# Optimization experiments

Measured on AMD Instinct MI355X. Metric: run time of the kernel, lower is better.

## Reference

```python
import jax, jax.numpy as jnp
import numpy as np
from jax import lax

# Static model/config sizes
B, ANG, C, H, NF, NB = 1, 9, 3, 128, 16, 2


def get_freq_position(n):
    """Anti-diagonal frequency bands of an n x n angular-DCT grid (python/static)."""
    bands = []
    for i in range(n):
        bands.append(([i], [0]))
    for j in range(1, n):
        bands.append(([n - 1], [j]))
    for item in bands:
        while item[0][0] > 0 and item[1][0] < n - 1:
            item[0].insert(0, item[0][0] - 1)
            item[1].insert(0, item[1][0] + 1)
    return bands


def dct_mat(n):
    """Orthonormal DCT-II matrix (row k = k-th basis)."""
    k = jnp.arange(n, dtype=jnp.float32)[:, None]
    i = jnp.arange(n, dtype=jnp.float32)[None, :]
    m = jnp.cos(jnp.pi * (i + 0.5) * k / n) * jnp.sqrt(2.0 / n)
    return m.at[0].multiply(1.0 / np.sqrt(2.0))


def conv3d(x, w, b):
    # x: (N, Cin, D, H, W), w: (Cout, Cin, 3, 3, 3)
    y = lax.conv_general_dilated(x, w, (1, 1, 1), 'SAME',
                                 dimension_numbers=('NCDHW', 'OIDHW', 'NCDHW'))
    return y + b[None, :, None, None, None]


def branch(cut, wi, bi, a, wb, bb):
    """init conv + NB ResBlock3D (PReLU -> Conv3d, residual), plus outer skip."""
    y0 = conv3d(cut, wi, bi)
    y = y0
    for k in range(NB):
        r = jnp.where(y >= 0, y, a[k] * y)  # PReLU (single-parameter)
        y = y + conv3d(r, wb[k], bb[k])
    return y0 + y


def setup_inputs() -> dict:
    key = jax.random.key(0)
    ks = jax.random.split(key, 32)

    def nrm(k, shape, s=0.05):
        return jax.random.normal(k, shape, dtype=jnp.float32) * s

    inp = {"x": jax.random.normal(ks[0], (B, ANG, ANG, C, H, H), dtype=jnp.float32)}
    i = 1
    for n in ("dc", "lo", "mi", "hi"):
        inp[f"w_{n}_i"] = nrm(ks[i], (NF, C, 3, 3, 3)); i += 1
        inp[f"b_{n}_i"] = nrm(ks[i], (NF,)); i += 1
        inp[f"a_{n}"] = jnp.full((NB,), 0.25, dtype=jnp.float32)
        inp[f"w_{n}"] = nrm(ks[i], (NB, NF, NF, 3, 3, 3)); i += 1
        inp[f"b_{n}"] = nrm(ks[i], (NB, NF)); i += 1
    inp["w_last"] = nrm(ks[i], (C, NF))  # 1x1 Conv2d, no bias
    return inp


def reference(x, w_dc_i, b_dc_i, a_dc, w_dc, b_dc,
              w_lo_i, b_lo_i, a_lo, w_lo, b_lo,
              w_mi_i, b_mi_i, a_mi, w_mi, b_mi,
              w_hi_i, b_hi_i, a_hi, w_hi, b_hi, w_last):
    b, u, v, c, h, w = x.shape
    Da = dct_mat(u)  # angular DCT (u == v)
    Ds = dct_mat(h)  # spatial DCT (h == w)

    # SpaAngDCT: spatial 2D DCT then angular 2D DCT
    xf = jnp.einsum('buvchw,Hh,Ww->buvcHW', x, Ds, Ds)
    xf = jnp.einsum('buvchw,Uu,Vv->bUVchw', xf, Da, Da)

    x_rec = jnp.zeros((b, NF, u, v, h, w), dtype=x.dtype)
    for idx, (ui, vi) in enumerate(get_freq_position(u)):
        if idx == 0:
            p = (w_dc_i, b_dc_i, a_dc, w_dc, b_dc)
        elif idx <= 2:
            p = (w_lo_i, b_lo_i, a_lo, w_lo, b_lo)
        elif idx <= u - 1:
            p = (w_mi_i, b_mi_i, a_mi, w_mi, b_mi)
        else:
            p = (w_hi_i, b_hi_i, a_hi, w_hi, b_hi)
        ua, va = jnp.array(ui), jnp.array(vi)
        cut = xf[:, ua, va].transpose(0, 2, 1, 3, 4)  # (b, c, L, h, w)
        out = branch(cut, *p)                          # (b, NF, L, h, w)
        x_rec = x_rec.at[:, :, ua, va].set(out)        # scatter band back

    # 'b c u v h w -> b c (u h) (v w)' then 1x1 conv (NF -> 3)
    xr = x_rec.transpose(0, 1, 2, 4, 3, 5).reshape(b, NF, u * h, v * w)
    xr = jnp.einsum('bnHW,on->boHW', xr, w_last)
    xr = xr.reshape(b, c, u, h, v, w).transpose(0, 2, 4, 1, 3, 5)  # (b,u,v,c,h,w)

    # InverseSpaAngDCT: angular IDCT then spatial IDCT
    xr = jnp.einsum('bUVchw,Uu,Vv->buvchw', xr, Da, Da)
    xr = jnp.einsum('buvcHW,Hh,Ww->buvchw', xr, Ds, Ds)
    return xr + x
```

## Files before the change

### kernel.cpp

```cpp
#include <hip/hip_runtime.h>
#include <hip/hip_bf16.h>
#include <math.h>

typedef __hip_bfloat16 bf16;
typedef __attribute__((ext_vector_type(8))) short short8;
typedef __attribute__((ext_vector_type(4))) float floatx4;
typedef __attribute__((ext_vector_type(4))) unsigned int uint4v;
typedef __attribute__((ext_vector_type(2))) unsigned int uint2v;

#define HW 16384
#define NSLICE 243

__constant__ int c_s_of_p[81] = {
  0, 1,1, 2,2,2, 3,3,3,3, 4,4,4,4,4, 5,5,5,5,5,5, 6,6,6,6,6,6,6,
  7,7,7,7,7,7,7,7, 8,8,8,8,8,8,8,8,8, 9,9,9,9,9,9,9,9,
  10,10,10,10,10,10,10, 11,11,11,11,11,11, 12,12,12,12,12,
  13,13,13,13, 14,14,14, 15,15, 16};
__constant__ int c_l_of_p[81] = {
  0, 0,1, 0,1,2, 0,1,2,3, 0,1,2,3,4, 0,1,2,3,4,5, 0,1,2,3,4,5,6,
  0,1,2,3,4,5,6,7, 0,1,2,3,4,5,6,7,8, 0,1,2,3,4,5,6,7,
  0,1,2,3,4,5,6, 0,1,2,3,4,5, 0,1,2,3,4, 0,1,2,3, 0,1,2, 0,1, 0};
__constant__ int c_L_of_s[17] = {1,2,3,4,5,6,7,8,9,8,7,6,5,4,3,2,1};
__constant__ int c_g_of_s[17] = {0,1,1,2,2,2,2,2,2,3,3,3,3,3,3,3,3};
__constant__ int c_pos_uv[81] = {
  0,1,3,6,10,15,21,28,36,
  2,4,7,11,16,22,29,37,45,
  5,8,12,17,23,30,38,46,53,
  9,13,18,24,31,39,47,54,60,
  14,19,25,32,40,48,55,61,66,
  20,26,33,41,49,56,62,67,71,
  27,34,42,50,57,63,68,72,75,
  35,43,51,58,64,69,73,76,78,
  44,52,59,65,70,74,77,79,80};

struct WPtrs {
  const float* wi[4]; const float* bi[4]; const float* a[4];
  const float* wb[4]; const float* bb[4]; const float* wl;
};

__device__ __forceinline__ unsigned short f2bf(float f) {
  return __bfloat16_as_ushort(__float2bfloat16(f));
}
__device__ __forceinline__ float bflo(unsigned int w) {
  return __uint_as_float(w << 16);
}
__device__ __forceinline__ float bfhi(unsigned int w) {
  return __uint_as_float(w & 0xffff0000u);
}
__device__ __forceinline__ unsigned int pack2(float a, float b) {
  return (unsigned int)f2bf(a) | ((unsigned int)f2bf(b) << 16);
}
__device__ __forceinline__ float invprelu(float v, float invA) {
  return (v >= 0.f) ? v : v * invA;
}
__device__ __forceinline__ void bfsplit(float v, unsigned short& hi, unsigned short& lo) {
  unsigned int bits = __float_as_uint(v);
  hi = (unsigned short)(bits >> 16);
  lo = f2bf(v - __uint_as_float(bits & 0xffff0000u));
}
__device__ __forceinline__ void gl_lds16(const void* g, void* l) {
  __builtin_amdgcn_global_load_lds(
      (const __attribute__((address_space(1))) unsigned int*)g,
      (__attribute__((address_space(3))) unsigned int*)l, 16, 0, 0);
}

__global__ __launch_bounds__(256) void k_setup(float* DaF,
                                               unsigned short* TFhi, unsigned short* TFlo,
                                               unsigned short* TIhi, unsigned short* TIlo) {
  const double PI = 3.14159265358979323846;
  int t = blockIdx.x * 256 + threadIdx.x;
  if (t < 81) {
    int U = t / 9, u = t % 9;
    double d = cos(PI * (u + 0.5) * U / 9.0) * sqrt(2.0 / 9.0);
    if (U == 0) d *= (1.0 / sqrt(2.0));
    DaF[t] = (float)d;
  }
  if (t < 16384) {
    int jj = t & 7, lane = (t >> 3) & 63, ks = (t >> 9) & 3, tile = t >> 11;
    int row = tile * 16 + (lane & 15);
    int colk = ks * 32 + (lane >> 4) * 8 + jj;
    double vF = cos(PI * (colk + 0.5) * row / 128.0) * sqrt(2.0 / 128.0);
    if (row == 0) vF *= (1.0 / sqrt(2.0));
    double vI = cos(PI * (row + 0.5) * colk / 128.0) * sqrt(2.0 / 128.0);
    if (colk == 0) vI *= (1.0 / sqrt(2.0));
    unsigned short h, l;
    bfsplit((float)vF, h, l); TFhi[t] = h; TFlo[t] = l;
    bfsplit((float)vI, h, l); TIhi[t] = h; TIlo[t] = l;
  }
}

__global__ __launch_bounds__(256) void k_prep(WPtrs P, unsigned short* Wmf,
                                              float* BiF, float* BbF,
                                              float* AF, float* WlF) {
  int t = blockIdx.x * 256 + threadIdx.x;
  if (t < 92160) {
    int s = t / 7680, r = t % 7680;
    int step = r / 512, r2 = r % 512;
    int lane = r2 >> 3, j = r2 & 7;
    int d = step / 5, i = step % 5;
    int q = lane >> 4, m = lane & 15;
    int tl = 2 * i + (q >> 1);
    int cin = (q & 1) * 8 + j;
    float val = 0.f;
    if (tl <= 8) {
      int ky = tl / 3, kx = tl % 3;
      int tap = d * 9 + ky * 3 + kx;
      if (s < 4) {
        if (cin < 3) val = P.wi[s][(m * 3 + cin) * 27 + tap];
      } else {
        int g = (s - 4) >> 1, k = (s - 4) & 1;
        val = P.wb[g][((k * 16 + m) * 16 + cin) * 27 + tap];
      }
    }
    Wmf[t] = f2bf(val);
  }
  if (t < 64)  BiF[t] = P.bi[t / 16][t % 16];
  if (t < 128) BbF[t] = P.bb[t / 32][t % 32];
  if (t < 8)   AF[t]  = P.a[t / 2][t % 2];
  if (t < 48)  WlF[t] = P.wl[t];
}

__global__ __launch_bounds__(256) void k_dct2(const float* __restrict__ X,
                                              const unsigned short* __restrict__ tabhi,
                                              const unsigned short* __restrict__ tablo,
                                              const float* __restrict__ xres,
                                              float* __restrict__ Y) {
  __shared__ unsigned short sThi[128 * 136];
  __shared__ unsigned short sTlo[128 * 136];
  int s = blockIdx.x;
  int t = threadIdx.x;
  int lane = t & 63, wv = t >> 6;
  int q = lane >> 4, n16 = lane & 15;
  const float* Xs = X + (size_t)s * HW;

  floatx4 acc[2][8];
#pragma unroll
  for (int mt = 0; mt < 2; mt++)
#pragma unroll
    for (int nt = 0; nt < 8; nt++) acc[mt][nt] = (floatx4){0.f, 0.f, 0.f, 0.f};

#pragma unroll
  for (int ks = 0; ks < 4; ks++) {
    short8 ahi[2], alo[2];
#pragma unroll
    for (int mt = 0; mt < 2; mt++) {
      const float* xp = Xs + (wv * 32 + mt * 16 + n16) * 128 + ks * 32 + q * 8;
      float4 a = *(const float4*)xp;
      float4 b = *(const float4*)(xp + 4);
      union { short8 v; unsigned short u[8]; } H, L;
      float xv[8] = {a.x, a.y, a.z, a.w, b.x, b.y, b.z, b.w};
#pragma unroll
      for (int j = 0; j < 8; j++) bfsplit(xv[j], H.u[j], L.u[j]);
      ahi[mt] = H.v; alo[mt] = L.v;
    }
#pragma unroll
    for (int nt = 0; nt < 8; nt++) {
      int e = nt * 2048 + ks * 512 + lane * 8;
      short8 bh = *(const short8*)(tabhi + e);
      short8 bl = *(const short8*)(tablo + e);
#pragma unroll
      for (int mt = 0; mt < 2; mt++) {
        acc[mt][nt] = __builtin_amdgcn_mfma_f32_16x16x32_bf16(ahi[mt], bl, acc[mt][nt], 0, 0, 0);
        acc[mt][nt] = __builtin_amdgcn_mfma_f32_16x16x32_bf16(alo[mt], bh, acc[mt][nt], 0, 0, 0);
        acc[mt][nt] = __builtin_amdgcn_mfma_f32_16x16x32_bf16(ahi[mt], bh, acc[mt][nt], 0, 0, 0);
      }
    }
  }

#pragma unroll
  for (int mt = 0; mt < 2; mt++)
#pragma unroll
    for (int nt = 0; nt < 8; nt++) {
      int col = nt * 16 + n16;
      int rowb = wv * 32 + mt * 16 + q * 4;
#pragma unroll
      for (int rp = 0; rp < 4; rp += 2) {
        unsigned short h0, l0, h1, l1;
        bfsplit(acc[mt][nt][rp], h0, l0);
        bfsplit(acc[mt][nt][rp + 1], h1, l1);
        int widx = (col * 136 + rowb + rp) >> 1;
        ((unsigned int*)sThi)[widx] = (unsigned int)h0 | ((unsigned int)h1 << 16);
        ((unsigned int*)sTlo)[widx] = (unsigned int)l0 | ((unsigned int)l1 << 16);
      }
    }
  __syncthreads();

#pragma unroll
  for (int mt = 0; mt < 2; mt++)
#pragma unroll
    for (int nt = 0; nt < 8; nt++) acc[mt][nt] = (floatx4){0.f, 0.f, 0.f, 0.f};

#pragma unroll
  for (int ks = 0; ks < 4; ks++) {
    short8 ahi[2], alo[2];
#pragma unroll
    for (int mt = 0; mt < 2; mt++) {
      int e = (wv * 2 + mt) * 2048 + ks * 512 + lane * 8;
      ahi[mt] = *(const short8*)(tabhi + e);
      alo[mt] = *(const short8*)(tablo + e);
    }
#pragma unroll
    for (int nt = 0; nt < 8; nt++) {
      int off = (nt * 16 + n16) * 136 + ks * 32 + q * 8;
      short8 bh = *(const short8*)(sThi + off);
      short8 bl = *(const short8*)(sTlo + off);
#pragma unroll
      for (int mt = 0; mt < 2; mt++) {
        acc[mt][nt] = __builtin_amdgcn_mfma_f32_16x16x32_bf16(ahi[mt], bl, acc[mt][nt], 0, 0, 0);
        acc[mt][nt] = __builtin_amdgcn_mfma_f32_16x16x32_bf16(alo[mt], bh, acc[mt][nt], 0, 0, 0);
        acc[mt][nt] = __builtin_amdgcn_mfma_f32_16x16x32_bf16(ahi[mt], bh, acc[mt][nt], 0, 0, 0);
      }
    }
  }

#pragma unroll
  for (int mt = 0; mt < 2; mt++)
#pragma unroll
    for (int nt = 0; nt < 8; nt++) {
      int row0 = wv * 32 + mt * 16 + q * 4;
      int col = nt * 16 + n16;
#pragma unroll
      for (int r = 0; r < 4; r++) {
        size_t oi = (size_t)s * HW + (size_t)(row0 + r) * 128 + col;
        float v = acc[mt][nt][r];
        if (xres) v += xres[oi];
        Y[oi] = v;
      }
    }
}

__global__ __launch_bounds__(128) void k_angF(const float* __restrict__ xf1,
                                              const float* __restrict__ DaF,
                                              unsigned short* __restrict__ xf2b) {
  __shared__ float L[81 * 128];
  __shared__ float sDa[81];
  int t = threadIdx.x;
  int c = blockIdx.y;
  int hw = blockIdx.x * 128 + t;
  if (t < 81) sDa[t] = DaF[t];
  __syncthreads();
#pragma unroll 3
  for (int i = 0; i < 81; i++)
    L[i * 128 + t] = xf1[(size_t)(i * 3 + c) * HW + hw];
  for (int v = 0; v < 9; v++) {
    float f[9];
#pragma unroll
    for (int u = 0; u < 9; u++) f[u] = L[(u * 9 + v) * 128 + t];
#pragma unroll
    for (int U = 0; U < 9; U++) {
      float a = 0.f;
#pragma unroll
      for (int u = 0; u < 9; u++) a += sDa[U * 9 + u] * f[u];
      L[(U * 9 + v) * 128 + t] = a;
    }
  }
  for (int U = 0; U < 9; U++) {
    float f[9];
#pragma unroll
    for (int v = 0; v < 9; v++) f[v] = L[(U * 9 + v) * 128 + t];
#pragma unroll
    for (int V = 0; V < 9; V++) {
      float a = 0.f;
#pragma unroll
      for (int v = 0; v < 9; v++) a += sDa[V * 9 + v] * f[v];
      size_t base = ((size_t)c_pos_uv[U * 9 + V] * HW + hw) * 4;
      xf2b[base + c] = f2bf(a);
      if (c == 0) xf2b[base + 3] = 0;
    }
  }
}

__global__ __launch_bounds__(128) void k_angI(const float* __restrict__ xrb,
                                              const float* __restrict__ DaF,
                                              float* __restrict__ xr2) {
  __shared__ float L[81 * 128];
  __shared__ float sDa[81];
  int t = threadIdx.x;
  int c = blockIdx.y;
  int hw = blockIdx.x * 128 + t;
  if (t < 81) sDa[t] = DaF[t];
  __syncthreads();
#pragma unroll 3
  for (int i = 0; i < 81; i++)
    L[i * 128 + t] = xrb[((size_t)c_pos_uv[i] * 3 + c) * HW + hw];
  for (int U = 0; U < 9; U++) {
    float f[9];
#pragma unroll
    for (int V = 0; V < 9; V++) f[V] = L[(U * 9 + V) * 128 + t];
#pragma unroll
    for (int v = 0; v < 9; v++) {
      float a = 0.f;
#pragma unroll
      for (int V = 0; V < 9; V++) a += sDa[V * 9 + v] * f[V];
      L[(U * 9 + v) * 128 + t] = a;
    }
  }
  for (int v = 0; v < 9; v++) {
    float f[9];
#pragma unroll
    for (int U = 0; U < 9; U++) f[U] = L[(U * 9 + v) * 128 + t];
#pragma unroll
    for (int u = 0; u < 9; u++) {
      float a = 0.f;
#pragma unroll
      for (int U = 0; U < 9; U++) a += sDa[U * 9 + u] * f[U];
      xr2[(size_t)((u * 9 + v) * 3 + c) * HW + hw] = a;
    }
  }
}

__global__ __launch_bounds__(512) void k_conv(const unsigned short* __restrict__ src,
                                              const unsigned short* __restrict__ prevAct,
                                              const unsigned short* __restrict__ act0,
                                              const unsigned short* __restrict__ Wmf,
                                              const float* __restrict__ BiF,
                                              const float* __restrict__ BbF,
                                              const float* __restrict__ AF,
                                              const float* __restrict__ WlF,
                                              int sel,
                                              unsigned short* __restrict__ boutAct,
                                              float* __restrict__ xrbOut) {
  __shared__ unsigned short s_lds[10 * 132 * 16];
  int p = blockIdx.y;
  int s = c_s_of_p[p], l = c_l_of_p[p];
  int g = c_g_of_s[s], Ls = c_L_of_s[s];
  int row0 = blockIdx.x * 8;
  int t = threadIdx.x;
  int lane = t & 63, wv = t >> 6;
  int q = lane >> 4, n = lane & 15;

  float aNext = (sel < 2) ? AF[g * 2 + sel] : 0.f;
  float invA  = (sel > 0) ? 1.0f / AF[g * 2 + sel - 1] : 0.f;

  int scol = t & 127;
  int shalf = (t >> 7) & 1;
  int srow0 = t >> 8;

  {
    uint4v z = (uint4v){0u, 0u, 0u, 0u};
    int zmax = (sel == 0) ? 1320 : 40;
    for (int i = t; i < zmax; i += 512) {
      int row, half, col;
      if (i < 40) { row = i >> 2; half = (i >> 1) & 1; col = (i & 1) ? 129 : 0; }
      else { int j = i - 40; row = j >> 7; col = (j & 127) + 1; half = 1; }
      *(uint4v*)((char*)s_lds + (size_t)(((row * 2 + half) * 132 + col)) * 16) = z;
    }
    for (int row = 0; row < 10; row++) {
      int grow = row0 - 1 + row;
      if ((unsigned)grow >= 128u) {
        for (int i = t; i < 264; i += 512) {
          int half = i / 132, col = i % 132;
          *(uint4v*)((char*)s_lds + (size_t)((row * 2 + half) * 132 + col) * 16) = z;
        }
      }
    }
  }

  int basel = wv * 4224 + (q & 1) * 2112 + n * 16;
  int off2[5];
#pragma unroll
  for (int i = 0; i < 5; i++) {
    int tl = 2 * i + (q >> 1);
    if (tl > 8) tl = 8;
    int ky = tl / 3, kx = tl % 3;
    off2[i] = basel + ky * 4224 + kx * 16;
  }

  int setIdx = (sel == 0) ? g : (4 + g * 2 + (sel - 1));
  const char* WsetBase = (const char*)Wmf + (size_t)setIdx * 15 * 1024;

  floatx4 acc[8];
#pragma unroll
  for (int cg = 0; cg < 8; cg++) acc[cg] = (floatx4){0.f, 0.f, 0.f, 0.f};

  for (int d = 0; d < 3; d++) {
    int l2 = l + d - 1;
    if (l2 < 0 || l2 >= Ls) continue;
    int p2 = p + d - 1;
    __syncthreads();
    if (sel == 0) {
      if (shalf == 0) {
#pragma unroll
        for (int it = 0; it < 5; it++) {
          int row = srow0 + it * 2;
          int grow = row0 - 1 + row;
          if ((unsigned)grow < 128u) {
            uint2v v2 = *(const uint2v*)(src + ((size_t)p2 * HW + grow * 128 + scol) * 4);
            uint4v val; val.x = v2.x; val.y = v2.y; val.z = 0u; val.w = 0u;
            *(uint4v*)((char*)s_lds + (size_t)((row * 2) * 132 + scol + 1) * 16) = val;
          }
        }
      }
    } else {
#pragma unroll
      for (int it = 0; it < 5; it++) {
        int row = srow0 + it * 2;
        int grow = row0 - 1 + row;
        if ((unsigned)grow < 128u) {
          const void* gp = (const void*)(src +
              (((size_t)p2 * HW + (size_t)grow * 128 + scol) * 16 + shalf * 8));
          void* lp = (void*)((char*)s_lds +
              (size_t)((row * 2 + shalf) * 132 + (wv & 1) * 64 + 1) * 16);
          gl_lds16(gp, lp);
        }
      }
    }
    __syncthreads();
    short8 af[5];
#pragma unroll
    for (int i = 0; i < 5; i++)
      af[i] = *(const short8*)(WsetBase + ((d * 5 + i) * 64 + lane) * 16);
#pragma unroll
    for (int cg = 0; cg < 8; cg++) {
#pragma unroll
      for (int i = 0; i < 5; i++) {
        short8 b = *(const short8*)((const char*)s_lds + off2[i] + cg * 256);
        acc[cg] = __builtin_amdgcn_mfma_f32_16x16x32_bf16(af[i], b, acc[cg], 0, 0, 0);
      }
    }
  }

  const float* bp = (sel == 0) ? (BiF + g * 16) : (BbF + g * 32 + (sel - 1) * 16);
  float bz[4];
#pragma unroll
  for (int r = 0; r < 4; r++) bz[r] = bp[q * 4 + r];
  int h = row0 + wv;

  if (sel < 2) {
#pragma unroll
    for (int cg = 0; cg < 8; cg++) {
      size_t pix = (size_t)p * HW + h * 128 + cg * 16 + n;
      float r0 = acc[cg][0] + bz[0], r1 = acc[cg][1] + bz[1];
      float r2 = acc[cg][2] + bz[2], r3 = acc[cg][3] + bz[3];
      if (sel != 0) {
        uint2v pv = *(const uint2v*)(prevAct + pix * 16 + q * 4);
        r0 += invprelu(bflo(pv.x), invA); r1 += invprelu(bfhi(pv.x), invA);
        r2 += invprelu(bflo(pv.y), invA); r3 += invprelu(bfhi(pv.y), invA);
      }
      r0 = fmaxf(r0, 0.f) + aNext * fminf(r0, 0.f);
      r1 = fmaxf(r1, 0.f) + aNext * fminf(r1, 0.f);
      r2 = fmaxf(r2, 0.f) + aNext * fminf(r2, 0.f);
      r3 = fmaxf(r3, 0.f) + aNext * fminf(r3, 0.f);
      uint2v ov; ov.x = pack2(r0, r1); ov.y = pack2(r2, r3);
      *(uint2v*)(boutAct + pix * 16 + q * 4) = ov;
    }
  } else {
    float invA0 = 1.0f / AF[g * 2];
    float wl0[4], wl1[4], wl2[4];
#pragma unroll
    for (int r = 0; r < 4; r++) {
      wl0[r] = WlF[q * 4 + r];
      wl1[r] = WlF[16 + q * 4 + r];
      wl2[r] = WlF[32 + q * 4 + r];
    }
#pragma unroll
    for (int cg = 0; cg < 8; cg++) {
      size_t pix = (size_t)p * HW + h * 128 + cg * 16 + n;
      float r0 = acc[cg][0] + bz[0], r1 = acc[cg][1] + bz[1];
      float r2 = acc[cg][2] + bz[2], r3 = acc[cg][3] + bz[3];
      uint2v pv = *(const uint2v*)(prevAct + pix * 16 + q * 4);
      r0 += invprelu(bflo(pv.x), invA); r1 += invprelu(bfhi(pv.x), invA);
      r2 += invprelu(bflo(pv.y), invA); r3 += invprelu(bfhi(pv.y), invA);
      uint2v p0 = *(const uint2v*)(act0 + pix * 16 + q * 4);
      r0 += invprelu(bflo(p0.x), invA0); r1 += invprelu(bfhi(p0.x), invA0);
      r2 += invprelu(bflo(p0.y), invA0); r3 += invprelu(bfhi(p0.y), invA0);
      float o0 = wl0[0] * r0 + wl0[1] * r1 + wl0[2] * r2 + wl0[3] * r3;
      float o1 = wl1[0] * r0 + wl1[1] * r1 + wl1[2] * r2 + wl1[3] * r3;
      float o2 = wl2[0] * r0 + wl2[1] * r1 + wl2[2] * r2 + wl2[3] * r3;
      o0 += __shfl_xor(o0, 16); o0 += __shfl_xor(o0, 32);
      o1 += __shfl_xor(o1, 16); o1 += __shfl_xor(o1, 32);
      o2 += __shfl_xor(o2, 16); o2 += __shfl_xor(o2, 32);
      if (q == 0) {
        size_t hw = (size_t)h * 128 + cg * 16 + n;
        xrbOut[((size_t)p * 3 + 0) * HW + hw] = o0;
        xrbOut[((size_t)p * 3 + 1) * HW + hw] = o1;
        xrbOut[((size_t)p * 3 + 2) * HW + hw] = o2;
      }
    }
  }
}

extern "C" void kernel_launch(void* const* d_in, const int* in_sizes, int n_in,
                              void* d_out, int out_size, void* d_ws, size_t ws_size,
                              hipStream_t stream) {
  (void)in_sizes; (void)n_in; (void)out_size; (void)ws_size;
  const float* x = (const float*)d_in[0];
  WPtrs P;
  for (int g = 0; g < 4; g++) {
    int b = 1 + g * 5;
    P.wi[g] = (const float*)d_in[b + 0];
    P.bi[g] = (const float*)d_in[b + 1];
    P.a[g]  = (const float*)d_in[b + 2];
    P.wb[g] = (const float*)d_in[b + 3];
    P.bb[g] = (const float*)d_in[b + 4];
  }
  P.wl = (const float*)d_in[21];

  char* base = (char*)d_ws;
  size_t off = 0;
  auto take = [&](size_t bytes) -> char* {
    char* r = base + off;
    off += (bytes + 255) & ~(size_t)255;
    return r;
  };
  float* DaF = (float*)take(81 * 4);
  unsigned short* TFhi = (unsigned short*)take(16384 * 2);
  unsigned short* TFlo = (unsigned short*)take(16384 * 2);
  unsigned short* TIhi = (unsigned short*)take(16384 * 2);
  unsigned short* TIlo = (unsigned short*)take(16384 * 2);
  unsigned short* Wmf = (unsigned short*)take(92160 * 2);
  float* BiF   = (float*)take(256);
  float* BbF   = (float*)take(512);
  float* AF    = (float*)take(32);
  float* WlF   = (float*)take(192);
  float* R1 = (float*)take((size_t)NSLICE * HW * 4);
  float* R3 = (float*)take((size_t)NSLICE * HW * 4);
  unsigned short* braw0 = (unsigned short*)take((size_t)81 * 16 * HW * 2);
  unsigned short* braw1 = (unsigned short*)take((size_t)81 * 16 * HW * 2);
  unsigned short* xf2b = (unsigned short*)R3;
  float* xrb = R3;

  k_setup<<<64, 256, 0, stream>>>(DaF, TFhi, TFlo, TIhi, TIlo);
  k_prep<<<360, 256, 0, stream>>>(P, Wmf, BiF, BbF, AF, WlF);
  k_dct2<<<243, 256, 0, stream>>>(x, TFhi, TFlo, nullptr, R1);
  k_angF<<<dim3(128, 3), 128, 0, stream>>>(R1, DaF, xf2b);
  k_conv<<<dim3(16, 81), 512, 0, stream>>>(xf2b, nullptr, nullptr, Wmf,
                                           BiF, BbF, AF, WlF, 0, braw0, nullptr);
  k_conv<<<dim3(16, 81), 512, 0, stream>>>(braw0, braw0, nullptr, Wmf,
                                           BiF, BbF, AF, WlF, 1, braw1, nullptr);
  k_conv<<<dim3(16, 81), 512, 0, stream>>>(braw1, braw1, braw0, Wmf,
                                           BiF, BbF, AF, WlF, 2, nullptr, xrb);
  k_angI<<<dim3(128, 3), 128, 0, stream>>>(xrb, DaF, R1);
  k_dct2<<<243, 256, 0, stream>>>(R1, TIhi, TIlo, x, (float*)d_out);
}
```

Measured before the change: 301.7 us.

## Merge setup kernels, bf16 intermediates, swizzle conv LDS, restructure angular DCT kernels

Merges the setup and weight-prep kernels into one launch. The forward spatial DCT now writes bf16 output, which the angular DCT reads directly from global memory instead of staging fp32 through LDS. The angular kernels use 256 threads and keep bf16 intermediates in LDS. The conv kernel gets a padded and swizzled LDS layout to reduce bank conflicts, and its weight-fragment loads are hoisted ahead of the tile fill. The extra bf16 rounding in the angular stages adds precision loss.

Result: faster. 294.8 us (-2.3%).

```diff
diff --git a/kernel.cpp b/kernel.cpp
--- a/kernel.cpp
+++ b/kernel.cpp
@@ -41,6 +41,9 @@
 __device__ __forceinline__ unsigned short f2bf(float f) {
   return __bfloat16_as_ushort(__float2bfloat16(f));
 }
+__device__ __forceinline__ float bf2f(unsigned short u) {
+  return __uint_as_float(((unsigned int)u) << 16);
+}
 __device__ __forceinline__ float bflo(unsigned int w) {
   return __uint_as_float(w << 16);
 }
@@ -63,10 +66,16 @@
       (const __attribute__((address_space(1))) unsigned int*)g,
       (__attribute__((address_space(3))) unsigned int*)l, 16, 0, 0);
 }
-
-__global__ __launch_bounds__(256) void k_setup(float* DaF,
-                                               unsigned short* TFhi, unsigned short* TFlo,
-                                               unsigned short* TIhi, unsigned short* TIlo) {
+__device__ __forceinline__ int ldsoff(int plane, int col) {
+  return plane * 2112 + ((plane & 3) << 5) + (col << 4);
+}
+
+__global__ __launch_bounds__(256) void k_init(WPtrs P, float* DaF,
+                                              unsigned short* TFhi, unsigned short* TFlo,
+                                              unsigned short* TIhi, unsigned short* TIlo,
+                                              unsigned short* Wmf,
+                                              float* BiF, float* BbF,
+                                              float* AF, float* WlF) {
   const double PI = 3.14159265358979323846;
   int t = blockIdx.x * 256 + threadIdx.x;
   if (t < 81) {
@@ -87,12 +96,6 @@
     bfsplit((float)vF, h, l); TFhi[t] = h; TFlo[t] = l;
     bfsplit((float)vI, h, l); TIhi[t] = h; TIlo[t] = l;
   }
-}
-
-__global__ __launch_bounds__(256) void k_prep(WPtrs P, unsigned short* Wmf,
-                                              float* BiF, float* BbF,
-                                              float* AF, float* WlF) {
-  int t = blockIdx.x * 256 + threadIdx.x;
   if (t < 92160) {
     int s = t / 7680, r = t % 7680;
     int step = r / 512, r2 = r % 512;
@@ -124,7 +127,8 @@
                                               const unsigned short* __restrict__ tabhi,
                                               const unsigned short* __restrict__ tablo,
                                               const float* __restrict__ xres,
-                                              float* __restrict__ Y) {
+                                              float* __restrict__ Yf,
+                                              unsigned short* __restrict__ Ybf) {
   __shared__ unsigned short sThi[128 * 136];
   __shared__ unsigned short sTlo[128 * 136];
   int s = blockIdx.x;
@@ -223,41 +227,43 @@
       for (int r = 0; r < 4; r++) {
         size_t oi = (size_t)s * HW + (size_t)(row0 + r) * 128 + col;
         float v = acc[mt][nt][r];
-        if (xres) v += xres[oi];
-        Y[oi] = v;
-      }
-    }
-}
-
-__global__ __launch_bounds__(128) void k_angF(const float* __restrict__ xf1,
-                                              const float* __restrict__ DaF,
-                                              unsigned short* __restrict__ xf2b) {
-  __shared__ float L[81 * 128];
+        if (Ybf) {
+          Ybf[oi] = f2bf(v);
+        } else {
+          if (xres) v += xres[oi];
+          Yf[oi] = v;
+        }
+      }
+    }
+}
+
+__global__ __launch_bounds__(256) void k_angF2(const unsigned short* __restrict__ in,
+                                               const float* __restrict__ DaF,
+                                               unsigned short* __restrict__ xf2b) {
+  __shared__ unsigned short L[81 * 256];
   __shared__ float sDa[81];
   int t = threadIdx.x;
   int c = blockIdx.y;
-  int hw = blockIdx.x * 128 + t;
+  int hw = blockIdx.x * 256 + t;
   if (t < 81) sDa[t] = DaF[t];
   __syncthreads();
-#pragma unroll 3
-  for (int i = 0; i < 81; i++)
-    L[i * 128 + t] = xf1[(size_t)(i * 3 + c) * HW + hw];
   for (int v = 0; v < 9; v++) {
     float f[9];
 #pragma unroll
-    for (int u = 0; u < 9; u++) f[u] = L[(u * 9 + v) * 128 + t];
+    for (int u = 0; u < 9; u++)
+      f[u] = bf2f(in[(size_t)((u * 9 + v) * 3 + c) * HW + hw]);
 #pragma unroll
     for (int U = 0; U < 9; U++) {
       float a = 0.f;
 #pragma unroll
       for (int u = 0; u < 9; u++) a += sDa[U * 9 + u] * f[u];
-      L[(U * 9 + v) * 128 + t] = a;
+      L[(U * 9 + v) * 256 + t] = f2bf(a);
     }
   }
   for (int U = 0; U < 9; U++) {
     float f[9];
 #pragma unroll
-    for (int v = 0; v < 9; v++) f[v] = L[(U * 9 + v) * 128 + t];
+    for (int v = 0; v < 9; v++) f[v] = bf2f(L[(U * 9 + v) * 256 + t]);
 #pragma unroll
     for (int V = 0; V < 9; V++) {
       float a = 0.f;
@@ -270,35 +276,33 @@
   }
 }
 
-__global__ __launch_bounds__(128) void k_angI(const float* __restrict__ xrb,
-                                              const float* __restrict__ DaF,
-                                              float* __restrict__ xr2) {
-  __shared__ float L[81 * 128];
+__global__ __launch_bounds__(256) void k_angI2(const float* __restrict__ xrb,
+                                               const float* __restrict__ DaF,
+                                               float* __restrict__ xr2) {
+  __shared__ unsigned short L[81 * 256];
   __shared__ float sDa[81];
   int t = threadIdx.x;
   int c = blockIdx.y;
-  int hw = blockIdx.x * 128 + t;
+  int hw = blockIdx.x * 256 + t;
   if (t < 81) sDa[t] = DaF[t];
   __syncthreads();
-#pragma unroll 3
-  for (int i = 0; i < 81; i++)
-    L[i * 128 + t] = xrb[((size_t)c_pos_uv[i] * 3 + c) * HW + hw];
   for (int U = 0; U < 9; U++) {
     float f[9];
 #pragma unroll
-    for (int V = 0; V < 9; V++) f[V] = L[(U * 9 + V) * 128 + t];
+    for (int V = 0; V < 9; V++)
+      f[V] = xrb[((size_t)c_pos_uv[U * 9 + V] * 3 + c) * HW + hw];
 #pragma unroll
     for (int v = 0; v < 9; v++) {
       float a = 0.f;
 #pragma unroll
       for (int V = 0; V < 9; V++) a += sDa[V * 9 + v] * f[V];
-      L[(U * 9 + v) * 128 + t] = a;
+      L[(U * 9 + v) * 256 + t] = f2bf(a);
     }
   }
   for (int v = 0; v < 9; v++) {
     float f[9];
 #pragma unroll
-    for (int U = 0; U < 9; U++) f[U] = L[(U * 9 + v) * 128 + t];
+    for (int U = 0; U < 9; U++) f[U] = bf2f(L[(U * 9 + v) * 256 + t]);
 #pragma unroll
     for (int u = 0; u < 9; u++) {
       float a = 0.f;
@@ -320,7 +324,7 @@
                                               int sel,
                                               unsigned short* __restrict__ boutAct,
                                               float* __restrict__ xrbOut) {
-  __shared__ unsigned short s_lds[10 * 132 * 16];
+  __shared__ unsigned short s_lds[21184];
   int p = blockIdx.y;
   int s = c_s_of_p[p], l = c_l_of_p[p];
   int g = c_g_of_s[s], Ls = c_L_of_s[s];
@@ -343,27 +347,26 @@
       int row, half, col;
       if (i < 40) { row = i >> 2; half = (i >> 1) & 1; col = (i & 1) ? 129 : 0; }
       else { int j = i - 40; row = j >> 7; col = (j & 127) + 1; half = 1; }
-      *(uint4v*)((char*)s_lds + (size_t)(((row * 2 + half) * 132 + col)) * 16) = z;
+      *(uint4v*)((char*)s_lds + ldsoff(row * 2 + half, col)) = z;
     }
     for (int row = 0; row < 10; row++) {
       int grow = row0 - 1 + row;
       if ((unsigned)grow >= 128u) {
         for (int i = t; i < 264; i += 512) {
           int half = i / 132, col = i % 132;
-          *(uint4v*)((char*)s_lds + (size_t)((row * 2 + half) * 132 + col) * 16) = z;
+          *(uint4v*)((char*)s_lds + ldsoff(row * 2 + half, col)) = z;
         }
       }
     }
   }
 
-  int basel = wv * 4224 + (q & 1) * 2112 + n * 16;
   int off2[5];
 #pragma unroll
   for (int i = 0; i < 5; i++) {
     int tl = 2 * i + (q >> 1);
     if (tl > 8) tl = 8;
     int ky = tl / 3, kx = tl % 3;
-    off2[i] = basel + ky * 4224 + kx * 16;
+    off2[i] = ldsoff(2 * (wv + ky) + (q & 1), n + kx);
   }
 
   int setIdx = (sel == 0) ? g : (4 + g * 2 + (sel - 1));
@@ -378,6 +381,10 @@
     if (l2 < 0 || l2 >= Ls) continue;
     int p2 = p + d - 1;
     __syncthreads();
+    short8 af[5];
+#pragma unroll
+    for (int i = 0; i < 5; i++)
+      af[i] = *(const short8*)(WsetBase + ((d * 5 + i) * 64 + lane) * 16);
     if (sel == 0) {
       if (shalf == 0) {
 #pragma unroll
@@ -387,7 +394,7 @@
           if ((unsigned)grow < 128u) {
             uint2v v2 = *(const uint2v*)(src + ((size_t)p2 * HW + grow * 128 + scol) * 4);
             uint4v val; val.x = v2.x; val.y = v2.y; val.z = 0u; val.w = 0u;
-            *(uint4v*)((char*)s_lds + (size_t)((row * 2) * 132 + scol + 1) * 16) = val;
+            *(uint4v*)((char*)s_lds + ldsoff(row * 2, scol + 1)) = val;
           }
         }
       }
@@ -400,16 +407,12 @@
           const void* gp = (const void*)(src +
               (((size_t)p2 * HW + (size_t)grow * 128 + scol) * 16 + shalf * 8));
           void* lp = (void*)((char*)s_lds +
-              (size_t)((row * 2 + shalf) * 132 + (wv & 1) * 64 + 1) * 16);
+              ldsoff(row * 2 + shalf, (wv & 1) * 64 + 1));
           gl_lds16(gp, lp);
         }
       }
     }
     __syncthreads();
-    short8 af[5];
-#pragma unroll
-    for (int i = 0; i < 5; i++)
-      af[i] = *(const short8*)(WsetBase + ((d * 5 + i) * 64 + lane) * 16);
 #pragma unroll
     for (int cg = 0; cg < 8; cg++) {
 #pragma unroll
@@ -514,22 +517,23 @@
   float* AF    = (float*)take(32);
   float* WlF   = (float*)take(192);
   float* R1 = (float*)take((size_t)NSLICE * HW * 4);
+  unsigned short* B1 = (unsigned short*)take((size_t)NSLICE * HW * 2);
   float* R3 = (float*)take((size_t)NSLICE * HW * 4);
   unsigned short* braw0 = (unsigned short*)take((size_t)81 * 16 * HW * 2);
   unsigned short* braw1 = (unsigned short*)take((size_t)81 * 16 * HW * 2);
   unsigned short* xf2b = (unsigned short*)R3;
   float* xrb = R3;
 
-  k_setup<<<64, 256, 0, stream>>>(DaF, TFhi, TFlo, TIhi, TIlo);
-  k_prep<<<360, 256, 0, stream>>>(P, Wmf, BiF, BbF, AF, WlF);
-  k_dct2<<<243, 256, 0, stream>>>(x, TFhi, TFlo, nullptr, R1);
-  k_angF<<<dim3(128, 3), 128, 0, stream>>>(R1, DaF, xf2b);
+  k_init<<<360, 256, 0, stream>>>(P, DaF, TFhi, TFlo, TIhi, TIlo,
+                                  Wmf, BiF, BbF, AF, WlF);
+  k_dct2<<<243, 256, 0, stream>>>(x, TFhi, TFlo, nullptr, nullptr, B1);
+  k_angF2<<<dim3(64, 3), 256, 0, stream>>>(B1, DaF, xf2b);
   k_conv<<<dim3(16, 81), 512, 0, stream>>>(xf2b, nullptr, nullptr, Wmf,
                                            BiF, BbF, AF, WlF, 0, braw0, nullptr);
   k_conv<<<dim3(16, 81), 512, 0, stream>>>(braw0, braw0, nullptr, Wmf,
                                            BiF, BbF, AF, WlF, 1, braw1, nullptr);
   k_conv<<<dim3(16, 81), 512, 0, stream>>>(braw1, braw1, braw0, Wmf,
                                            BiF, BbF, AF, WlF, 2, nullptr, xrb);
-  k_angI<<<dim3(128, 3), 128, 0, stream>>>(xrb, DaF, R1);
-  k_dct2<<<243, 256, 0, stream>>>(R1, TIhi, TIlo, x, (float*)d_out);
-}
+  k_angI2<<<dim3(64, 3), 256, 0, stream>>>(xrb, DaF, R1);
+  k_dct2<<<243, 256, 0, stream>>>(R1, TIhi, TIlo, x, (float*)d_out, nullptr);
+}
```
